# Kernel tuning notes

Measured on AMD Instinct MI355X. Metric: run time of the kernel, lower is better.

## Reference

```python
import jax, jax.numpy as jnp
import numpy as np

B, N, C = 8, 2048, 512

def setup_inputs() -> dict:
    key = jax.random.key(0)
    k1, k2, k3 = jax.random.split(key, 3)
    x = jax.random.normal(k1, (B, N, C), dtype=jnp.float32)
    # xavier_uniform with gain=1.414 ~ uniform(-b, b), b = gain*sqrt(6/(fan_in+fan_out))
    bw = 1.414 * np.sqrt(6.0 / (C + C))
    w = jax.random.uniform(k2, (C, C), dtype=jnp.float32, minval=-bw, maxval=bw)
    ba = 1.414 * np.sqrt(6.0 / (2 * C + 1))
    a = jax.random.uniform(k3, (2 * C, 1), dtype=jnp.float32, minval=-ba, maxval=ba)
    return {"x": x, "w": w, "a": a}

def reference(x, w, a):
    # x: [B,N,C], w: [C,C], a: [2C,1]
    C_ = w.shape[0]
    h = jnp.matmul(x, w)                      # [B,N,C]
    a1 = a[:C_, 0]                            # [C]
    a2 = a[C_:, 0]                            # [C]
    # The torch repeat/cat/view builds e_ij = LeakyReLU(a1.h_i + a2.h_j);
    # compute the same math via broadcasting (no [B,N,N,2C] tensor).
    s1 = jnp.einsum('bnc,c->bn', h, a1)       # [B,N]
    s2 = jnp.einsum('bnc,c->bn', h, a2)       # [B,N]
    e = jax.nn.leaky_relu(s1[:, :, None] + s2[:, None, :], negative_slope=0.2)  # [B,N,N]
    attention = jax.nn.softmax(e, axis=2)     # softmax over source nodes j
    # dropout is identity in eval mode (training=False)
    h_prime = jnp.matmul(attention, x)        # [B,N,C]
    return h_prime
```

## Files before the change

kernel.cpp:

```cpp
#include <hip/hip_runtime.h>
#include <math.h>

#define B_ 8
#define N_ 2048
#define C_ 512
#define G_ 64
#define L_ 32

static const size_t OFF_V1   = 0;
static const size_t OFF_V2   = OFF_V1 + 512;
static const size_t OFF_S1   = OFF_V2 + 512;
static const size_t OFF_S2   = OFF_S1 + 16384;
static const size_t OFF_Z    = OFF_S2 + 16384;
static const size_t OFF_IDX  = OFF_Z + 16384;
static const size_t OFF_P    = OFF_IDX + 16384;
static const size_t OFF_Q    = OFF_P + 16384;
static const size_t OFF_CHP  = OFF_Q + 16384;
static const size_t OFF_CHQ  = OFF_CHP + 262144;
static const size_t OFF_TOTQ = OFF_CHQ + 262144;
static const size_t OFF_EMR  = OFF_TOTQ + 4096;
static const size_t OFF_EMP  = OFF_EMR + 16384;
static const size_t OFF_EMQ  = OFF_EMP + 16384;
static const size_t OFF_POS  = OFF_EMQ + 16384;

__global__ __launch_bounds__(64) void k_wa(const float* __restrict__ w,
                                           const float* __restrict__ a,
                                           float* __restrict__ v1, float* __restrict__ v2) {
    int k = blockIdx.x, lane = threadIdx.x;
    float acc1 = 0.f, acc2 = 0.f;
    for (int c = lane; c < C_; c += 64) {
        float wv = w[k * C_ + c];
        acc1 += wv * a[c];
        acc2 += wv * a[C_ + c];
    }
    for (int o = 32; o > 0; o >>= 1) { acc1 += __shfl_down(acc1, o); acc2 += __shfl_down(acc2, o); }
    if (lane == 0) { v1[k] = acc1; v2[k] = acc2; }
}

__global__ __launch_bounds__(256) void k_s(const float* __restrict__ x,
                                           const float* __restrict__ v1,
                                           const float* __restrict__ v2,
                                           float* __restrict__ s1, float* __restrict__ s2) {
    __shared__ __align__(16) float sv1[C_];
    __shared__ __align__(16) float sv2[C_];
    int tid = threadIdx.x;
    for (int c = tid; c < C_; c += 256) { sv1[c] = v1[c]; sv2[c] = v2[c]; }
    __syncthreads();
    int wave = tid >> 6, lane = tid & 63;
    int r = blockIdx.x * 4 + wave;
    const float4* xr  = reinterpret_cast<const float4*>(x + (size_t)r * C_);
    const float4* w1p = reinterpret_cast<const float4*>(sv1);
    const float4* w2p = reinterpret_cast<const float4*>(sv2);
    float a1 = 0.f, a2 = 0.f;
    #pragma unroll
    for (int half = 0; half < 2; ++half) {
        int c4 = lane + half * 64;
        float4 xv = xr[c4], w1 = w1p[c4], w2 = w2p[c4];
        a1 += xv.x*w1.x + xv.y*w1.y + xv.z*w1.z + xv.w*w1.w;
        a2 += xv.x*w2.x + xv.y*w2.y + xv.z*w2.z + xv.w*w2.w;
    }
    for (int o = 32; o > 0; o >>= 1) { a1 += __shfl_down(a1, o); a2 += __shfl_down(a2, o); }
    if (lane == 0) { s1[r] = a1; s2[r] = a2; }
}

__global__ __launch_bounds__(256) void k_rank(const float* __restrict__ s2,
                                              float* __restrict__ z, int* __restrict__ idxArr,
                                              float* __restrict__ pArr, float* __restrict__ qArr) {
    __shared__ float sval[N_];
    __shared__ float sred[256];
    __shared__ int   srnk[256];
    int blk = blockIdx.x;
    int b = blk >> 5, grp = blk & 31;
    int tid = threadIdx.x;
    int le = tid & 63, qtr = tid >> 6;
    for (int i = tid; i < N_; i += 256) sval[i] = s2[(size_t)b * N_ + i];
    __syncthreads();
    int e = grp * 64 + le;
    float val = sval[e];
    int base = qtr * 512;
    int rank = 0;
    float mx = -3.4e38f;
    #pragma unroll 8
    for (int i = 0; i < 512; ++i) {
        int t = base + i;
        float v = sval[t];
        mx = fmaxf(mx, v);
        rank += (v < val) || (v == val && t < e);
    }
    srnk[tid] = rank;
    sred[tid] = mx;
    __syncthreads();
    for (int o = 128; o > 0; o >>= 1) {
        if (tid < o) sred[tid] = fmaxf(sred[tid], sred[tid + o]);
        __syncthreads();
    }
    float m2 = sred[0];
    if (qtr == 0) {
        int rk = srnk[le] + srnk[le + 64] + srnk[le + 128] + srnk[le + 192];
        float d = val - m2;
        size_t pos = (size_t)b * N_ + rk;
        z[pos]      = val;
        idxArr[pos] = e;
        pArr[pos]   = __expf(d);
        qArr[pos]   = __expf(0.2f * d);
    }
}

__global__ __launch_bounds__(512) void k_chunk(const float* __restrict__ x,
                                               const int* __restrict__ idxArr,
                                               const float* __restrict__ pArr,
                                               const float* __restrict__ qArr,
                                               float* __restrict__ chP, float* __restrict__ chQ) {
    int bg = blockIdx.x, b = bg >> 6, g = bg & 63;
    int c = threadIdx.x;
    __shared__ int   srow[L_];
    __shared__ float spv[L_], sqv[L_];
    if (c < L_) {
        int j = g * L_ + c;
        srow[c] = idxArr[b * N_ + j];
        spv[c]  = pArr[b * N_ + j];
        sqv[c]  = qArr[b * N_ + j];
    }
    __syncthreads();
    const float* xb = x + (size_t)b * N_ * C_;
    float xr_[L_];
    #pragma unroll
    for (int t = 0; t < L_; ++t) xr_[t] = xb[(size_t)srow[t] * C_ + c];
    float accP = 0.f, accQ = 0.f;
    #pragma unroll
    for (int t = 0; t < L_; ++t) {
        accP = fmaf(spv[t], xr_[t], accP);
        accQ = fmaf(sqv[t], xr_[t], accQ);
    }
    chP[(size_t)bg * C_ + c] = accP;
    chQ[(size_t)bg * C_ + c] = accQ;
}

__global__ __launch_bounds__(1024) void k_prep(const float* __restrict__ s1,
                                               const float* __restrict__ z,
                                               const float* __restrict__ pArr,
                                               const float* __restrict__ qArr,
                                               float* __restrict__ chP,
                                               float* __restrict__ chQ,
                                               float* __restrict__ totQ,
                                               int* __restrict__ emRow,
                                               float* __restrict__ emFP,
                                               float* __restrict__ emFQ,
                                               int* __restrict__ posStart) {
    __shared__ float Ppre[2049], Qpre[2049];
    __shared__ float zv[N_];
    __shared__ int   cnt[2049];
    __shared__ int   ps[2050];
    __shared__ float wsP[16], wsQ[16], woP[16], woQ[16];
    __shared__ int   wsC[16], woC[16];
    int b = blockIdx.x, tid = threadIdx.x, lane = tid & 63, wid = tid >> 6;
    size_t ib = (size_t)b * N_;

    for (int i = tid; i < 2049; i += 1024) cnt[i] = 0;
    zv[2*tid]   = z[ib + 2*tid];
    zv[2*tid+1] = z[ib + 2*tid+1];

    float p0 = pArr[ib + 2*tid], p1 = pArr[ib + 2*tid+1];
    float q0 = qArr[ib + 2*tid], q1 = qArr[ib + 2*tid+1];
    float pv = p0 + p1, qv = q0 + q1;
    float pi = pv, qi = qv;
    for (int o = 1; o < 64; o <<= 1) {
        float tp = __shfl_up(pi, o), tq2 = __shfl_up(qi, o);
        if (lane >= o) { pi += tp; qi += tq2; }
    }
    if (lane == 63) { wsP[wid] = pi; wsQ[wid] = qi; }
    __syncthreads();
    if (wid == 0 && lane < 16) {
        float sp = wsP[lane], sq = wsQ[lane];
        float ip = sp, iq = sq;
        for (int o = 1; o < 16; o <<= 1) {
            float tp = __shfl_up(ip, o), tq2 = __shfl_up(iq, o);
            if (lane >= o) { ip += tp; iq += tq2; }
        }
        woP[lane] = ip - sp; woQ[lane] = iq - sq;
    }
    {
        int c = tid & 511, sel = tid >> 9;
        float* arr = sel ? chQ : chP;
        float v[G_];
        #pragma unroll
        for (int g = 0; g < G_; ++g)
            v[g] = arr[((size_t)(b * G_ + g)) * C_ + c];
        float run = 0.f;
        #pragma unroll
        for (int g = G_ - 1; g >= 0; --g) {
            float t = v[g];
            arr[((size_t)(b * G_ + g)) * C_ + c] = run;
            run += t;
        }
        if (sel) totQ[b * C_ + c] = run;
    }
    __syncthreads();
    float inclP = pi + woP[wid], inclQ = qi + woQ[wid];
    float exclP = inclP - pv,    exclQ = inclQ - qv;
    Ppre[2*tid]   = exclP;  Ppre[2*tid+1] = exclP + p0;
    Qpre[2*tid]   = exclQ;  Qpre[2*tid+1] = exclQ + q0;
    if (tid == 1023) { Ppre[2048] = inclP; Qpre[2048] = inclQ; }
    __syncthreads();

    float m2   = zv[N_ - 1];
    float Ptot = Ppre[2048];
    int   kk[2], sl[2];
    float fPv[2], fQv[2];
    #pragma unroll
    for (int h = 0; h < 2; ++h) {
        int rl = tid + h * 1024;
        float s1v = s1[ib + rl];
        float thr = -s1v;
        int lo = 0, hi = N_;
        while (lo < hi) { int mid = (lo + hi) >> 1; if (zv[mid] >= thr) hi = mid; else lo = mid + 1; }
        float beta = s1v + m2;
        float wPc, wQc;
        if (beta >= 0.f) { wPc = 1.f;                  wQc = __expf(-0.8f * beta); }
        else             { wPc = __expf(0.8f * beta);  wQc = 1.f; }
        float Sp = Ptot - Ppre[lo];
        float Sq = Qpre[lo];
        float inv = 1.f / (wPc * Sp + wQc * Sq);
        fPv[h] = wPc * inv;
        fQv[h] = wQc * inv;
        kk[h] = lo;
        sl[h] = atomicAdd(&cnt[lo], 1);
    }
    __syncthreads();

    int c0 = cnt[2*tid], c1 = cnt[2*tid+1];
    int cv = c0 + c1, ci = cv;
    for (int o = 1; o < 64; o <<= 1) {
        int t = __shfl_up(ci, o);
        if (lane >= o) ci += t;
    }
    if (lane == 63) wsC[wid] = ci;
    __syncthreads();
    if (wid == 0 && lane < 16) {
        int sc = wsC[lane], ic = sc;
        for (int o = 1; o < 16; o <<= 1) { int t = __shfl_up(ic, o); if (lane >= o) ic += t; }
        woC[lane] = ic - sc;
    }
    __syncthreads();
    int inclC = ci + woC[wid];
    int exclC = inclC - cv;
    ps[2*tid] = exclC; ps[2*tid+1] = exclC + c0;
    if (tid == 1023) { ps[2048] = inclC; ps[2049] = inclC + cnt[2048]; }
    __syncthreads();
    posStart[b * 2050 + tid]        = ps[tid];
    posStart[b * 2050 + 1024 + tid] = ps[1024 + tid];
    if (tid < 2) posStart[b * 2050 + 2048 + tid] = ps[2048 + tid];
    #pragma unroll
    for (int h = 0; h < 2; ++h) {
        int rl = tid + h * 1024;
        int u  = ps[kk[h]] + sl[h];
        emRow[ib + u] = rl;
        emFP [ib + u] = fPv[h];
        emFQ [ib + u] = fQv[h];
    }
}

__global__ __launch_bounds__(512) void k_fused(const float* __restrict__ x,
                                               const int* __restrict__ idxArr,
                                               const float* __restrict__ pArr,
                                               const float* __restrict__ qArr,
                                               const float* __restrict__ chP,
                                               const float* __restrict__ chQ,
                                               const float* __restrict__ totQ,
                                               const int* __restrict__ emRow,
                                               const float* __restrict__ emFP,
                                               const float* __restrict__ emFQ,
                                               const int* __restrict__ posStart,
                                               float* __restrict__ out) {
    int bg = blockIdx.x, b = bg >> 6, g = bg & 63;
    int c = threadIdx.x;
    __shared__ int   srow[L_];
    __shared__ float spv[L_], sqv[L_];
    __shared__ int   sps[L_ + 2];
    __shared__ int   semRow[N_];
    __shared__ float semFP[N_], semFQ[N_];
    if (c < L_) {
        int j = g * L_ + c;
        srow[c] = idxArr[b * N_ + j];
        spv[c]  = pArr[b * N_ + j];
        sqv[c]  = qArr[b * N_ + j];
    }
    if (c < L_ + 2) sps[c] = posStart[b * 2050 + g * L_ + c];
    __syncthreads();
    int uStart = sps[0];
    int uEnd   = (g == G_ - 1) ? sps[L_ + 1] : sps[L_];
    size_t ib = (size_t)b * N_;
    for (int u = uStart + c; u < uEnd; u += 512) {
        int e = u - uStart;
        semRow[e] = emRow[ib + u];
        semFP[e]  = emFP [ib + u];
        semFQ[e]  = emFQ [ib + u];
    }
    __syncthreads();
    const float* xb = x + (size_t)b * N_ * C_;
    float*       ob = out + (size_t)b * N_ * C_;
    float xr_[L_];
    #pragma unroll
    for (int t = 0; t < L_; ++t) xr_[t] = xb[(size_t)srow[t] * C_ + c];
    float runP = chP[(size_t)bg * C_ + c];
    float runQ = chQ[(size_t)bg * C_ + c];
    float tq   = totQ[b * C_ + c];
    if (g == G_ - 1) {
        for (int u = sps[L_]; u < sps[L_ + 1]; ++u) {
            int e = u - uStart;
            ob[(size_t)semRow[e] * C_ + c] = semFP[e] * runP + semFQ[e] * (tq - runQ);
        }
    }
    #pragma unroll
    for (int t = L_ - 1; t >= 0; --t) {
        runP = fmaf(spv[t], xr_[t], runP);
        runQ = fmaf(sqv[t], xr_[t], runQ);
        for (int u = sps[t]; u < sps[t + 1]; ++u) {
            int e = u - uStart;
            ob[(size_t)semRow[e] * C_ + c] = semFP[e] * runP + semFQ[e] * (tq - runQ);
        }
    }
}

extern "C" void kernel_launch(void* const* d_in, const int* in_sizes, int n_in,
                              void* d_out, int out_size, void* d_ws, size_t ws_size,
                              hipStream_t stream) {
    const float* x = (const float*)d_in[0];
    const float* w = (const float*)d_in[1];
    const float* a = (const float*)d_in[2];
    float* out = (float*)d_out;
    float* ws  = (float*)d_ws;

    float* v1   = ws + OFF_V1;
    float* v2   = ws + OFF_V2;
    float* s1   = ws + OFF_S1;
    float* s2   = ws + OFF_S2;
    float* zArr = ws + OFF_Z;
    int*   idxA = (int*)(ws + OFF_IDX);
    float* pArr = ws + OFF_P;
    float* qArr = ws + OFF_Q;
    float* chP  = ws + OFF_CHP;
    float* chQ  = ws + OFF_CHQ;
    float* totQ = ws + OFF_TOTQ;
    int*   emR  = (int*)(ws + OFF_EMR);
    float* emP  = ws + OFF_EMP;
    float* emQ  = ws + OFF_EMQ;
    int*   pos  = (int*)(ws + OFF_POS);

    k_wa   <<<dim3(C_),      dim3(64),   0, stream>>>(w, a, v1, v2);
    k_s    <<<dim3(4096),    dim3(256),  0, stream>>>(x, v1, v2, s1, s2);
    k_rank <<<dim3(B_ * 32), dim3(256),  0, stream>>>(s2, zArr, idxA, pArr, qArr);
    k_chunk<<<dim3(B_ * G_), dim3(512),  0, stream>>>(x, idxA, pArr, qArr, chP, chQ);
    k_prep <<<dim3(B_),      dim3(1024), 0, stream>>>(s1, zArr, pArr, qArr, chP, chQ, totQ,
                                                      emR, emP, emQ, pos);
    k_fused<<<dim3(B_ * G_), dim3(512),  0, stream>>>(x, idxA, pArr, qArr, chP, chQ, totQ,
                                                      emR, emP, emQ, pos, out);
}
```

Before: 140.3 us.

## Vectorize chunk and fused kernels with float4 row-groups; split chunk prefix into kernel

k_chunk and k_fused now have each thread load float4 columns over an 8-row subgroup, with four row-groups per block. Partial sums are combined through shared memory, and in k_fused the suffix-sum offsets are rebuilt from the higher row-groups. The reverse chunk prefix over chP/chQ moves out of the 8-block k_prep into a separate 64-block k_choff kernel, so it runs across more blocks. The aim is wider memory transactions and more parallelism, at the cost of an extra launch, shared-memory reductions and more complex output ordering logic.

```diff
diff --git a/kernel.cpp b/kernel.cpp
--- a/kernel.cpp
+++ b/kernel.cpp
@@ -23,6 +23,21 @@
 static const size_t OFF_EMQ  = OFF_EMP + 16384;
 static const size_t OFF_POS  = OFF_EMQ + 16384;
 
+__device__ inline float4 f4z() { return make_float4(0.f, 0.f, 0.f, 0.f); }
+__device__ inline float4 fma4(float s, float4 a, float4 c) {
+    c.x = fmaf(s, a.x, c.x); c.y = fmaf(s, a.y, c.y);
+    c.z = fmaf(s, a.z, c.z); c.w = fmaf(s, a.w, c.w); return c;
+}
+__device__ inline float4 add4(float4 a, float4 b) {
+    return make_float4(a.x + b.x, a.y + b.y, a.z + b.z, a.w + b.w);
+}
+__device__ inline float4 comb4(float fp, float4 P, float fq, float4 T, float4 Q) {
+    return make_float4(fp * P.x + fq * (T.x - Q.x),
+                       fp * P.y + fq * (T.y - Q.y),
+                       fp * P.z + fq * (T.z - Q.z),
+                       fp * P.w + fq * (T.w - Q.w));
+}
+
 __global__ __launch_bounds__(64) void k_wa(const float* __restrict__ w,
                                            const float* __restrict__ a,
                                            float* __restrict__ v1, float* __restrict__ v2) {
@@ -112,37 +127,64 @@
                                                const float* __restrict__ qArr,
                                                float* __restrict__ chP, float* __restrict__ chQ) {
     int bg = blockIdx.x, b = bg >> 6, g = bg & 63;
-    int c = threadIdx.x;
+    int tid = threadIdx.x;
     __shared__ int   srow[L_];
     __shared__ float spv[L_], sqv[L_];
-    if (c < L_) {
-        int j = g * L_ + c;
-        srow[c] = idxArr[b * N_ + j];
-        spv[c]  = pArr[b * N_ + j];
-        sqv[c]  = qArr[b * N_ + j];
-    }
-    __syncthreads();
-    const float* xb = x + (size_t)b * N_ * C_;
-    float xr_[L_];
-    #pragma unroll
-    for (int t = 0; t < L_; ++t) xr_[t] = xb[(size_t)srow[t] * C_ + c];
-    float accP = 0.f, accQ = 0.f;
-    #pragma unroll
-    for (int t = 0; t < L_; ++t) {
-        accP = fmaf(spv[t], xr_[t], accP);
-        accQ = fmaf(sqv[t], xr_[t], accQ);
-    }
-    chP[(size_t)bg * C_ + c] = accP;
-    chQ[(size_t)bg * C_ + c] = accQ;
+    __shared__ float4 partP[4][128], partQ[4][128];
+    if (tid < L_) {
+        int j = g * L_ + tid;
+        srow[tid] = idxArr[b * N_ + j];
+        spv[tid]  = pArr[b * N_ + j];
+        sqv[tid]  = qArr[b * N_ + j];
+    }
+    __syncthreads();
+    int rg = tid >> 7, q = tid & 127;
+    const float4* xb4 = reinterpret_cast<const float4*>(x + (size_t)b * N_ * C_);
+    float4 aP = f4z(), aQ = f4z();
+    #pragma unroll
+    for (int i = 0; i < 8; ++i) {
+        int j = rg * 8 + i;
+        float4 xv = xb4[(size_t)srow[j] * 128 + q];
+        aP = fma4(spv[j], xv, aP);
+        aQ = fma4(sqv[j], xv, aQ);
+    }
+    partP[rg][q] = aP;
+    partQ[rg][q] = aQ;
+    __syncthreads();
+    if (tid < 128) {
+        float4 s = add4(add4(partP[0][tid], partP[1][tid]), add4(partP[2][tid], partP[3][tid]));
+        reinterpret_cast<float4*>(chP + (size_t)bg * C_)[tid] = s;
+    } else if (tid < 256) {
+        int qq = tid - 128;
+        float4 s = add4(add4(partQ[0][qq], partQ[1][qq]), add4(partQ[2][qq], partQ[3][qq]));
+        reinterpret_cast<float4*>(chQ + (size_t)bg * C_)[qq] = s;
+    }
+}
+
+__global__ __launch_bounds__(128) void k_choff(float* __restrict__ chP, float* __restrict__ chQ,
+                                               float* __restrict__ totQ) {
+    int t = blockIdx.x * 128 + threadIdx.x;
+    int isQ = t >> 12, rem = t & 4095;
+    int b = rem >> 9, c = rem & 511;
+    float* arr = isQ ? chQ : chP;
+    float v[G_];
+    #pragma unroll
+    for (int g = 0; g < G_; ++g)
+        v[g] = arr[((size_t)(b * G_ + g)) * C_ + c];
+    float run = 0.f;
+    #pragma unroll
+    for (int g = G_ - 1; g >= 0; --g) {
+        float tv = v[g];
+        arr[((size_t)(b * G_ + g)) * C_ + c] = run;
+        run += tv;
+    }
+    if (isQ) totQ[b * C_ + c] = run;
 }
 
 __global__ __launch_bounds__(1024) void k_prep(const float* __restrict__ s1,
                                                const float* __restrict__ z,
                                                const float* __restrict__ pArr,
                                                const float* __restrict__ qArr,
-                                               float* __restrict__ chP,
-                                               float* __restrict__ chQ,
-                                               float* __restrict__ totQ,
                                                int* __restrict__ emRow,
                                                float* __restrict__ emFP,
                                                float* __restrict__ emFQ,
@@ -178,22 +220,6 @@
             if (lane >= o) { ip += tp; iq += tq2; }
         }
         woP[lane] = ip - sp; woQ[lane] = iq - sq;
-    }
-    {
-        int c = tid & 511, sel = tid >> 9;
-        float* arr = sel ? chQ : chP;
-        float v[G_];
-        #pragma unroll
-        for (int g = 0; g < G_; ++g)
-            v[g] = arr[((size_t)(b * G_ + g)) * C_ + c];
-        float run = 0.f;
-        #pragma unroll
-        for (int g = G_ - 1; g >= 0; --g) {
-            float t = v[g];
-            arr[((size_t)(b * G_ + g)) * C_ + c] = run;
-            run += t;
-        }
-        if (sel) totQ[b * C_ + c] = run;
     }
     __syncthreads();
     float inclP = pi + woP[wid], inclQ = qi + woQ[wid];
@@ -231,14 +257,14 @@
     int c0 = cnt[2*tid], c1 = cnt[2*tid+1];
     int cv = c0 + c1, ci = cv;
     for (int o = 1; o < 64; o <<= 1) {
-        int t = __shfl_up(ci, o);
-        if (lane >= o) ci += t;
+        int t2 = __shfl_up(ci, o);
+        if (lane >= o) ci += t2;
     }
     if (lane == 63) wsC[wid] = ci;
     __syncthreads();
     if (wid == 0 && lane < 16) {
         int sc = wsC[lane], ic = sc;
-        for (int o = 1; o < 16; o <<= 1) { int t = __shfl_up(ic, o); if (lane >= o) ic += t; }
+        for (int o = 1; o < 16; o <<= 1) { int t2 = __shfl_up(ic, o); if (lane >= o) ic += t2; }
         woC[lane] = ic - sc;
     }
     __syncthreads();
@@ -273,51 +299,68 @@
                                                const int* __restrict__ posStart,
                                                float* __restrict__ out) {
     int bg = blockIdx.x, b = bg >> 6, g = bg & 63;
-    int c = threadIdx.x;
+    int tid = threadIdx.x;
     __shared__ int   srow[L_];
     __shared__ float spv[L_], sqv[L_];
     __shared__ int   sps[L_ + 2];
     __shared__ int   semRow[N_];
     __shared__ float semFP[N_], semFQ[N_];
-    if (c < L_) {
-        int j = g * L_ + c;
-        srow[c] = idxArr[b * N_ + j];
-        spv[c]  = pArr[b * N_ + j];
-        sqv[c]  = qArr[b * N_ + j];
-    }
-    if (c < L_ + 2) sps[c] = posStart[b * 2050 + g * L_ + c];
+    __shared__ float4 partP[4][128], partQ[4][128];
+    if (tid < L_) {
+        int j = g * L_ + tid;
+        srow[tid] = idxArr[b * N_ + j];
+        spv[tid]  = pArr[b * N_ + j];
+        sqv[tid]  = qArr[b * N_ + j];
+    }
+    if (tid >= 64 && tid < 64 + L_ + 2) sps[tid - 64] = posStart[b * 2050 + g * L_ + (tid - 64)];
     __syncthreads();
     int uStart = sps[0];
     int uEnd   = (g == G_ - 1) ? sps[L_ + 1] : sps[L_];
     size_t ib = (size_t)b * N_;
-    for (int u = uStart + c; u < uEnd; u += 512) {
+    for (int u = uStart + tid; u < uEnd; u += 512) {
         int e = u - uStart;
         semRow[e] = emRow[ib + u];
         semFP[e]  = emFP [ib + u];
         semFQ[e]  = emFQ [ib + u];
     }
-    __syncthreads();
-    const float* xb = x + (size_t)b * N_ * C_;
-    float*       ob = out + (size_t)b * N_ * C_;
-    float xr_[L_];
-    #pragma unroll
-    for (int t = 0; t < L_; ++t) xr_[t] = xb[(size_t)srow[t] * C_ + c];
-    float runP = chP[(size_t)bg * C_ + c];
-    float runQ = chQ[(size_t)bg * C_ + c];
-    float tq   = totQ[b * C_ + c];
-    if (g == G_ - 1) {
+    int rg = tid >> 7, q = tid & 127;
+    const float4* xb4 = reinterpret_cast<const float4*>(x + (size_t)b * N_ * C_);
+    float4 xr4[8];
+    #pragma unroll
+    for (int i = 0; i < 8; ++i)
+        xr4[i] = xb4[(size_t)srow[rg * 8 + i] * 128 + q];
+    float4 sP = f4z(), sQ = f4z();
+    #pragma unroll
+    for (int i = 0; i < 8; ++i) {
+        int j = rg * 8 + i;
+        sP = fma4(spv[j], xr4[i], sP);
+        sQ = fma4(sqv[j], xr4[i], sQ);
+    }
+    partP[rg][q] = sP;
+    partQ[rg][q] = sQ;
+    __syncthreads();
+    float4 runP = reinterpret_cast<const float4*>(chP + (size_t)bg * C_)[q];
+    float4 runQ = reinterpret_cast<const float4*>(chQ + (size_t)bg * C_)[q];
+    float4 tq4  = reinterpret_cast<const float4*>(totQ + (size_t)b * C_)[q];
+    #pragma unroll
+    for (int rg2 = 3; rg2 >= 1; --rg2) {
+        if (rg2 > rg) { runP = add4(runP, partP[rg2][q]); runQ = add4(runQ, partQ[rg2][q]); }
+    }
+    float4* ob4 = reinterpret_cast<float4*>(out + (size_t)b * N_ * C_);
+    if (g == G_ - 1 && rg == 3) {
         for (int u = sps[L_]; u < sps[L_ + 1]; ++u) {
             int e = u - uStart;
-            ob[(size_t)semRow[e] * C_ + c] = semFP[e] * runP + semFQ[e] * (tq - runQ);
+            ob4[(size_t)semRow[e] * 128 + q] = comb4(semFP[e], runP, semFQ[e], tq4, runQ);
         }
     }
     #pragma unroll
-    for (int t = L_ - 1; t >= 0; --t) {
-        runP = fmaf(spv[t], xr_[t], runP);
-        runQ = fmaf(sqv[t], xr_[t], runQ);
-        for (int u = sps[t]; u < sps[t + 1]; ++u) {
+    for (int t = 7; t >= 0; --t) {
+        int j = rg * 8 + t;
+        runP = fma4(spv[j], xr4[t], runP);
+        runQ = fma4(sqv[j], xr4[t], runQ);
+        for (int u = sps[j]; u < sps[j + 1]; ++u) {
             int e = u - uStart;
-            ob[(size_t)semRow[e] * C_ + c] = semFP[e] * runP + semFQ[e] * (tq - runQ);
+            ob4[(size_t)semRow[e] * 128 + q] = comb4(semFP[e], runP, semFQ[e], tq4, runQ);
         }
     }
 }
@@ -351,8 +394,8 @@
     k_s    <<<dim3(4096),    dim3(256),  0, stream>>>(x, v1, v2, s1, s2);
     k_rank <<<dim3(B_ * 32), dim3(256),  0, stream>>>(s2, zArr, idxA, pArr, qArr);
     k_chunk<<<dim3(B_ * G_), dim3(512),  0, stream>>>(x, idxA, pArr, qArr, chP, chQ);
-    k_prep <<<dim3(B_),      dim3(1024), 0, stream>>>(s1, zArr, pArr, qArr, chP, chQ, totQ,
-                                                      emR, emP, emQ, pos);
+    k_choff<<<dim3(64),      dim3(128),  0, stream>>>(chP, chQ, totQ);
+    k_prep <<<dim3(B_),      dim3(1024), 0, stream>>>(s1, zArr, pArr, qArr, emR, emP, emQ, pos);
     k_fused<<<dim3(B_ * G_), dim3(512),  0, stream>>>(x, idxA, pArr, qArr, chP, chQ, totQ,
                                                       emR, emP, emQ, pos, out);
 }
```

After: 133.0 us. -5.2%, faster.
